# Kernel tuning notes

Hardware: AMD Instinct MI355X
Metric: run time of the kernel (lower is better)

The kernel has to match this reference:

```python
import jax, jax.numpy as jnp
import numpy as np

B, N, D, H = 16, 512, 256, 8
DK = D // H
EPS = 1e-6
NEG_INF = 1e12
LAM_ATT, LAM_DIST, LAM_ADJ = 0.3, 0.3, 0.4


def setup_inputs() -> dict:
    key = jax.random.key(0)
    ks = jax.random.split(key, 16)
    inp = {
        "query": jax.random.normal(ks[0], (B, N, D), jnp.float32),
        "key": jax.random.normal(ks[1], (B, N, D), jnp.float32),
        "value": jax.random.normal(ks[2], (B, N, D), jnp.float32),
        "adj_matrix": jax.random.uniform(ks[3], (B, N, N), jnp.float32),
        "distances_matrix": jax.random.uniform(ks[4], (B, N, N), jnp.float32),
        "edges_att": jnp.zeros((1,), jnp.float32),
        "mask": jnp.ones((B, N), jnp.int32),
    }
    s = 1.0 / np.sqrt(D)
    # four Linear(d_model, d_model): Wq, Wk, Wv, Wo (+ biases)
    for i, nm in enumerate(["q", "k", "v", "o"]):
        inp[f"W{nm}"] = jax.random.normal(ks[5 + 2 * i], (D, D), jnp.float32) * s
        inp[f"b{nm}"] = jax.random.normal(ks[6 + 2 * i], (D,), jnp.float32) * s
    return inp


def _proj(x, W, b):
    # [B,N,D] -> [B,H,N,DK]
    y = x @ W.T + b
    return y.reshape(B, N, H, DK).transpose(0, 2, 1, 3)


def reference(query, key, value, adj_matrix, distances_matrix, edges_att, mask,
              Wq, bq, Wk, bk, Wv, bv, Wo, bo):
    q = _proj(query, Wq, bq)
    k = _proj(key, Wk, bk)
    v = _proj(value, Wv, bv)

    valid = mask != 0  # [B,N] key-side validity

    # distance kernel: softmax(-d) over keys, masked positions -> 0 prob
    d_scores = jnp.where(valid[:, None, :], -distances_matrix, -jnp.inf)
    p_dist = jax.nn.softmax(d_scores, axis=-1)  # [B,N,N]

    # scaled dot-product attention with key mask
    scores = jnp.einsum("bhqd,bhkd->bhqk", q, k) / np.sqrt(DK)
    scores = jnp.where(valid[:, None, None, :], scores, -NEG_INF)
    p_attn = jax.nn.softmax(scores, axis=-1)  # [B,H,N,N]

    # row-normalized adjacency
    p_adj = adj_matrix / (adj_matrix.sum(axis=-1, keepdims=True) + EPS)  # [B,N,N]

    # blend three attention terms (broadcast dist/adj over heads)
    p_weighted = (LAM_ATT * p_attn
                  + LAM_DIST * p_dist[:, None]
                  + LAM_ADJ * p_adj[:, None])  # [B,H,N,N]

    x = jnp.einsum("bhqk,bhkd->bhqd", p_weighted, v)  # [B,H,N,DK]
    x = x.transpose(0, 2, 1, 3).reshape(B, N, D)
    out = x @ Wo.T + bo  # output projection (4th linear)
    return out
```

## Files before the change

kernel.cpp:

```cpp
#include <hip/hip_runtime.h>
#include <cstdint>
#include <cstddef>

#define B_  16
#define N_  512
#define D_  256
#define H_  8
#define DK_ 32

#define QKV_ELEMS 2097152

__device__ __align__(16) unsigned short g_Qb[QKV_ELEMS];
__device__ __align__(16) unsigned short g_Kb[QKV_ELEMS];
__device__ __align__(16) unsigned short g_VT[QKV_ELEMS];
__device__ __align__(16) unsigned short g_STb[(size_t)B_*N_*N_];
__device__ __align__(16) unsigned short g_Wb[4*D_*D_];

typedef short v8s __attribute__((ext_vector_type(8)));
typedef float v4f __attribute__((ext_vector_type(4)));

__device__ __forceinline__ unsigned short f2b(float f){
  unsigned int x;
  __builtin_memcpy(&x, &f, 4);
  x = x + 0x7FFFu + ((x >> 16) & 1u);
  return (unsigned short)(x >> 16);
}

#if defined(__has_builtin)
#if __has_builtin(__builtin_amdgcn_cvt_pk_bf16_f32)
#define PK_BF16 1
#endif
#endif

__device__ __forceinline__ unsigned int pk2(float a, float b){
#ifdef PK_BF16
  typedef __bf16 v2bf __attribute__((ext_vector_type(2)));
  v2bf r = __builtin_amdgcn_cvt_pk_bf16_f32(a, b);
  unsigned int u;
  __builtin_memcpy(&u, &r, 4);
  return u;
#else
  return (unsigned int)f2b(a) | ((unsigned int)f2b(b) << 16);
#endif
}
__device__ __forceinline__ v8s pk8(const float4 a, const float4 b){
  union { unsigned int u[4]; v8s v; } x;
  x.u[0] = pk2(a.x, a.y); x.u[1] = pk2(a.z, a.w);
  x.u[2] = pk2(b.x, b.y); x.u[3] = pk2(b.z, b.w);
  return x.v;
}

__global__ __launch_bounds__(256) void conv_w(
    const float* __restrict__ Wq, const float* __restrict__ Wk,
    const float* __restrict__ Wv, const float* __restrict__ Wo)
{
  const int widx = blockIdx.x >> 6;
  const int i = ((blockIdx.x & 63)*256 + threadIdx.x)*4;
  const float* src = (widx==0) ? Wq : (widx==1) ? Wk : (widx==2) ? Wv : Wo;
  const float4 u = *reinterpret_cast<const float4*>(src + i);
  uint2 o2;
  o2.x = pk2(u.x, u.y);
  o2.y = pk2(u.z, u.w);
  *reinterpret_cast<uint2*>(g_Wb + widx*65536 + i) = o2;
}

__global__ __launch_bounds__(256) void fused_mid(
    const float* __restrict__ query, const float* __restrict__ key_,
    const float* __restrict__ value, const float* __restrict__ dist,
    const float* __restrict__ adjm,  const int* __restrict__ mask,
    const float* __restrict__ bq, const float* __restrict__ bk,
    const float* __restrict__ bv)
{
  const int bid = blockIdx.x;
  const int t   = threadIdx.x;
  const int w = t >> 6, lane = t & 63, kl = lane & 15, quad = lane >> 4;

  if (bid < 1536){
    const int z  = bid >> 9;
    const int rr = bid & 511;
    const int mt = rr >> 2, nt = rr & 3;
    const float* Ap = (z==0) ? query : (z==1) ? key_ : value;
    const float* bp = (z==0) ? bq : (z==1) ? bk : bv;
    const unsigned short* Wb = g_Wb + z*65536;
    const int m0 = mt*64 + w*16;
    const int n0 = nt*64;

    v4f acc[4];
    #pragma unroll
    for (int nb = 0; nb < 4; ++nb) acc[nb] = (v4f){0.f,0.f,0.f,0.f};
    const int arow = m0 + kl;

    if (z == 2){
      #pragma unroll
      for (int k0 = 0; k0 < 256; k0 += 32){
        const float* ap = Ap + (size_t)arow*256 + k0 + quad*8;
        const v8s af = pk8(reinterpret_cast<const float4*>(ap)[0],
                           reinterpret_cast<const float4*>(ap)[1]);
        #pragma unroll
        for (int nb = 0; nb < 4; ++nb){
          const v8s wf = *reinterpret_cast<const v8s*>(
              Wb + (size_t)(n0 + nb*16 + kl)*256 + k0 + quad*8);
          acc[nb] = __builtin_amdgcn_mfma_f32_16x16x32_bf16(wf, af, acc[nb], 0, 0, 0);
        }
      }
      const int tok = m0 + kl, bb = tok >> 9, nr = tok & 511;
      #pragma unroll
      for (int nb = 0; nb < 4; ++nb)
        #pragma unroll
        for (int r = 0; r < 4; ++r){
          const int n = n0 + nb*16 + quad*4 + r;
          const float v = acc[nb][r] + bp[n];
          g_VT[(((size_t)bb*H_ + (n>>5))*DK_ + (n&31))*N_ + nr] = f2b(v);
        }
    } else {
      #pragma unroll
      for (int k0 = 0; k0 < 256; k0 += 32){
        const float* ap = Ap + (size_t)arow*256 + k0 + quad*8;
        const v8s af = pk8(reinterpret_cast<const float4*>(ap)[0],
                           reinterpret_cast<const float4*>(ap)[1]);
        #pragma unroll
        for (int nb = 0; nb < 4; ++nb){
          const v8s wf = *reinterpret_cast<const v8s*>(
              Wb + (size_t)(n0 + nb*16 + kl)*256 + k0 + quad*8);
          acc[nb] = __builtin_amdgcn_mfma_f32_16x16x32_bf16(af, wf, acc[nb], 0, 0, 0);
        }
      }
      unsigned short* dst = z ? g_Kb : g_Qb;
      #pragma unroll
      for (int nb = 0; nb < 4; ++nb){
        const int n = n0 + nb*16 + kl;
        const float bias = bp[n];
        #pragma unroll
        for (int r = 0; r < 4; ++r){
          const int m = m0 + quad*4 + r;
          const float v = acc[nb][r] + bias;
          dst[(((size_t)(m>>9)*H_ + (n>>5))*N_ + (m&511))*DK_ + (n&31)] = f2b(v);
        }
      }
    }
    return;
  }

  {
    const int row = (bid - 1536)*4 + w;
    const int b   = row >> 9;
    const size_t roff = (size_t)row*N_ + lane*8;
    const float4 d0 = *reinterpret_cast<const float4*>(dist + roff);
    const float4 d1 = *reinterpret_cast<const float4*>(dist + roff + 4);
    const float4 a0 = *reinterpret_cast<const float4*>(adjm + roff);
    const float4 a1 = *reinterpret_cast<const float4*>(adjm + roff + 4);
    const int4   m0v = *reinterpret_cast<const int4*>(mask + b*N_ + lane*8);
    const int4   m1v = *reinterpret_cast<const int4*>(mask + b*N_ + lane*8 + 4);
    float e[8], a[8];
    e[0] = m0v.x ? __expf(-d0.x) : 0.f;  e[1] = m0v.y ? __expf(-d0.y) : 0.f;
    e[2] = m0v.z ? __expf(-d0.z) : 0.f;  e[3] = m0v.w ? __expf(-d0.w) : 0.f;
    e[4] = m1v.x ? __expf(-d1.x) : 0.f;  e[5] = m1v.y ? __expf(-d1.y) : 0.f;
    e[6] = m1v.z ? __expf(-d1.z) : 0.f;  e[7] = m1v.w ? __expf(-d1.w) : 0.f;
    a[0]=a0.x; a[1]=a0.y; a[2]=a0.z; a[3]=a0.w;
    a[4]=a1.x; a[5]=a1.y; a[6]=a1.z; a[7]=a1.w;
    float lz = 0.f, la = 0.f;
    #pragma unroll
    for (int i = 0; i < 8; ++i){ lz += e[i]; la += a[i]; }
    #pragma unroll
    for (int o = 1; o < 64; o <<= 1){
      lz += __shfl_xor(lz, o, 64);
      la += __shfl_xor(la, o, 64);
    }
    const float c0 = (lz > 0.f) ? 0.3f / lz : 0.f;
    const float c1 = 0.4f / (la + 1e-6f);
    uint4 o4;
    o4.x = pk2(e[0]*c0 + a[0]*c1, e[1]*c0 + a[1]*c1);
    o4.y = pk2(e[2]*c0 + a[2]*c1, e[3]*c0 + a[3]*c1);
    o4.z = pk2(e[4]*c0 + a[4]*c1, e[5]*c0 + a[5]*c1);
    o4.w = pk2(e[6]*c0 + a[6]*c1, e[7]*c0 + a[7]*c1);
    *reinterpret_cast<uint4*>(g_STb + roff) = o4;
  }
}

__global__ __launch_bounds__(512) void attn_kernel(
    const int* __restrict__ mask, const float* __restrict__ bo,
    float* __restrict__ out)
{
  __shared__ unsigned short Pl[8*2*640];
  __shared__ unsigned short Xl[16*264];
  const int bid = blockIdx.x;
  const int b  = bid & 15;
  const int qt = bid >> 4;
  const int q0 = qt*16;
  const int t  = threadIdx.x;
  const int w  = t >> 6, lane = t & 63;
  const int kl = lane & 15, quad = lane >> 4;
  const int h  = w;
  const size_t bh = (size_t)b*H_ + h;
  const float scale = 0.17677669529663687f;

  const unsigned short* Qp = g_Qb + (bh*N_ + q0)*DK_;
  const unsigned short* Kp = g_Kb + bh*N_*DK_;
  const unsigned short* Vp = g_VT + bh*DK_*N_;
  const unsigned short* Sp = g_STb + ((size_t)(b*N_ + q0))*N_;
  const int* mrow = mask + b*N_;
  const v4f vz = {0.f, 0.f, 0.f, 0.f};

  const v8s aq = *reinterpret_cast<const v8s*>(Qp + (size_t)kl*DK_ + quad*8);

  v4f acc[32];
  #pragma unroll
  for (int kb = 0; kb < 32; ++kb){
    const v8s ak = *reinterpret_cast<const v8s*>(Kp + (size_t)(kb*16 + kl)*DK_ + quad*8);
    acc[kb] = __builtin_amdgcn_mfma_f32_16x16x32_bf16(ak, aq, vz, 0, 0, 0);
  }

  float psum = 0.f;
  #pragma unroll
  for (int kb = 0; kb < 32; ++kb){
    const int4 mv = reinterpret_cast<const int4*>(mrow + kb*16)[quad];
    acc[kb][0] = mv.x ? __expf(acc[kb][0]*scale) : 0.f;
    acc[kb][1] = mv.y ? __expf(acc[kb][1]*scale) : 0.f;
    acc[kb][2] = mv.z ? __expf(acc[kb][2]*scale) : 0.f;
    acc[kb][3] = mv.w ? __expf(acc[kb][3]*scale) : 0.f;
    psum += (acc[kb][0] + acc[kb][1]) + (acc[kb][2] + acc[kb][3]);
  }
  psum += __shfl_xor(psum, 16, 64);
  psum += __shfl_xor(psum, 32, 64);
  const float inv = (psum > 0.f) ? 0.3f / psum : 0.f;

  unsigned short* Pw = Pl + w*1280;
  v4f o0 = vz, o1 = vz;
  #pragma unroll
  for (int c = 0; c < 16; ++c){
    unsigned short* Pb = Pw + (c & 1)*640;
    {
      union { unsigned int u[2]; unsigned long long ll; } p0, p1;
      p0.u[0] = pk2(acc[2*c  ][0]*inv, acc[2*c  ][1]*inv);
      p0.u[1] = pk2(acc[2*c  ][2]*inv, acc[2*c  ][3]*inv);
      p1.u[0] = pk2(acc[2*c+1][0]*inv, acc[2*c+1][1]*inv);
      p1.u[1] = pk2(acc[2*c+1][2]*inv, acc[2*c+1][3]*inv);
      *reinterpret_cast<unsigned long long*>(&Pb[kl*40 + quad*4])      = p0.ll;
      *reinterpret_cast<unsigned long long*>(&Pb[kl*40 + 16 + quad*4]) = p1.ll;
    }
    const v8s bp  = *reinterpret_cast<const v8s*>(&Pb[kl*40 + quad*8]);
    const v8s bst = *reinterpret_cast<const v8s*>(Sp + (size_t)kl*N_ + c*32 + quad*8);
    const v8s av0 = *reinterpret_cast<const v8s*>(Vp + (size_t)(     kl)*N_ + c*32 + quad*8);
    const v8s av1 = *reinterpret_cast<const v8s*>(Vp + (size_t)(16 + kl)*N_ + c*32 + quad*8);
    o0 = __builtin_amdgcn_mfma_f32_16x16x32_bf16(av0, bp,  o0, 0, 0, 0);
    o0 = __builtin_amdgcn_mfma_f32_16x16x32_bf16(av0, bst, o0, 0, 0, 0);
    o1 = __builtin_amdgcn_mfma_f32_16x16x32_bf16(av1, bp,  o1, 0, 0, 0);
    o1 = __builtin_amdgcn_mfma_f32_16x16x32_bf16(av1, bst, o1, 0, 0, 0);
  }

  {
    unsigned short* xr = Xl + kl*264 + h*32;
    *reinterpret_cast<unsigned int*>(&xr[quad*4])          = pk2(o0[0], o0[1]);
    *reinterpret_cast<unsigned int*>(&xr[quad*4 + 2])      = pk2(o0[2], o0[3]);
    *reinterpret_cast<unsigned int*>(&xr[16 + quad*4])     = pk2(o1[0], o1[1]);
    *reinterpret_cast<unsigned int*>(&xr[16 + quad*4 + 2]) = pk2(o1[2], o1[3]);
  }
  __syncthreads();

  {
    const unsigned short* WoB = g_Wb + 3*65536;
    const int n0 = w*32;
    v4f a20 = vz, a21 = vz;
    #pragma unroll
    for (int k0 = 0; k0 < 256; k0 += 32){
      const v8s af  = *reinterpret_cast<const v8s*>(&Xl[kl*264 + k0 + quad*8]);
      const v8s wf0 = *reinterpret_cast<const v8s*>(WoB + (size_t)(n0 + kl)*256 + k0 + quad*8);
      const v8s wf1 = *reinterpret_cast<const v8s*>(WoB + (size_t)(n0 + 16 + kl)*256 + k0 + quad*8);
      a20 = __builtin_amdgcn_mfma_f32_16x16x32_bf16(af, wf0, a20, 0, 0, 0);
      a21 = __builtin_amdgcn_mfma_f32_16x16x32_bf16(af, wf1, a21, 0, 0, 0);
    }
    const int n_0 = n0 + kl, n_1 = n0 + 16 + kl;
    const float b0v = bo[n_0], b1v = bo[n_1];
    #pragma unroll
    for (int r = 0; r < 4; ++r){
      const size_t m = (size_t)(b*N_ + q0 + quad*4 + r);
      out[m*256 + n_0] = a20[r] + b0v;
      out[m*256 + n_1] = a21[r] + b1v;
    }
  }
}

extern "C" void kernel_launch(void* const* d_in, const int* in_sizes, int n_in,
                              void* d_out, int out_size, void* d_ws, size_t ws_size,
                              hipStream_t stream)
{
  const float* query = (const float*)d_in[0];
  const float* key_  = (const float*)d_in[1];
  const float* value = (const float*)d_in[2];
  const float* adjm  = (const float*)d_in[3];
  const float* dist  = (const float*)d_in[4];
  const int*   mask  = (const int*)d_in[6];
  const float* Wq = (const float*)d_in[7];  const float* bq = (const float*)d_in[8];
  const float* Wk = (const float*)d_in[9];  const float* bk = (const float*)d_in[10];
  const float* Wv = (const float*)d_in[11]; const float* bv = (const float*)d_in[12];
  const float* Wo = (const float*)d_in[13]; const float* bo = (const float*)d_in[14];

  conv_w<<<256, 256, 0, stream>>>(Wq, Wk, Wv, Wo);
  fused_mid<<<3584, 256, 0, stream>>>(query, key_, value, dist, adjm, mask,
                                      bq, bk, bv);
  attn_kernel<<<512, 512, 0, stream>>>(mask, bo, (float*)d_out);
}
```

Measured before the change: 198.1 us.

## Drop weight-conversion kernel and stream attention softmax with hi/lo bf16 split

Removes the separate conv_w launch. Q/K/V weights are now read as fp32 and packed to bf16 inside the projection GEMM, and Wo conversion runs as extra blocks of fused_mid. In attn_kernel the 32-tile score array held in registers is replaced by a single streaming pass. Unnormalized exp scores are split into bf16 hi and lo parts and fed through extra MFMAs, with normalization applied at the end and the static term accumulated separately. This cuts a launch and register pressure at the cost of redundant weight conversion and more MFMA and LDS work per tile.

New measurement: 216.8 us. +9.5%, slower.

```diff
diff --git a/kernel.cpp b/kernel.cpp
--- a/kernel.cpp
+++ b/kernel.cpp
@@ -14,9 +14,10 @@
 __device__ __align__(16) unsigned short g_Kb[QKV_ELEMS];
 __device__ __align__(16) unsigned short g_VT[QKV_ELEMS];
 __device__ __align__(16) unsigned short g_STb[(size_t)B_*N_*N_];
-__device__ __align__(16) unsigned short g_Wb[4*D_*D_];
+__device__ __align__(16) unsigned short g_WoB[D_*D_];
 
 typedef short v8s __attribute__((ext_vector_type(8)));
+typedef short v4s __attribute__((ext_vector_type(4)));
 typedef float v4f __attribute__((ext_vector_type(4)));
 
 __device__ __forceinline__ unsigned short f2b(float f){
@@ -49,25 +50,21 @@
   x.u[2] = pk2(b.x, b.y); x.u[3] = pk2(b.z, b.w);
   return x.v;
 }
-
-__global__ __launch_bounds__(256) void conv_w(
-    const float* __restrict__ Wq, const float* __restrict__ Wk,
-    const float* __restrict__ Wv, const float* __restrict__ Wo)
-{
-  const int widx = blockIdx.x >> 6;
-  const int i = ((blockIdx.x & 63)*256 + threadIdx.x)*4;
-  const float* src = (widx==0) ? Wq : (widx==1) ? Wk : (widx==2) ? Wv : Wo;
-  const float4 u = *reinterpret_cast<const float4*>(src + i);
-  uint2 o2;
-  o2.x = pk2(u.x, u.y);
-  o2.y = pk2(u.z, u.w);
-  *reinterpret_cast<uint2*>(g_Wb + widx*65536 + i) = o2;
+__device__ __forceinline__ float lo16f(unsigned int u){
+  const unsigned int x = u << 16;
+  float f; __builtin_memcpy(&f, &x, 4); return f;
+}
+__device__ __forceinline__ float hi16f(unsigned int u){
+  const unsigned int x = u & 0xFFFF0000u;
+  float f; __builtin_memcpy(&f, &x, 4); return f;
 }
 
 __global__ __launch_bounds__(256) void fused_mid(
     const float* __restrict__ query, const float* __restrict__ key_,
     const float* __restrict__ value, const float* __restrict__ dist,
     const float* __restrict__ adjm,  const int* __restrict__ mask,
+    const float* __restrict__ Wq, const float* __restrict__ Wk,
+    const float* __restrict__ Wv, const float* __restrict__ Wo,
     const float* __restrict__ bq, const float* __restrict__ bk,
     const float* __restrict__ bv)
 {
@@ -80,8 +77,8 @@
     const int rr = bid & 511;
     const int mt = rr >> 2, nt = rr & 3;
     const float* Ap = (z==0) ? query : (z==1) ? key_ : value;
+    const float* Wp = (z==0) ? Wq : (z==1) ? Wk : Wv;
     const float* bp = (z==0) ? bq : (z==1) ? bk : bv;
-    const unsigned short* Wb = g_Wb + z*65536;
     const int m0 = mt*64 + w*16;
     const int n0 = nt*64;
 
@@ -90,19 +87,24 @@
     for (int nb = 0; nb < 4; ++nb) acc[nb] = (v4f){0.f,0.f,0.f,0.f};
     const int arow = m0 + kl;
 
+    #pragma unroll
+    for (int k0 = 0; k0 < 256; k0 += 32){
+      const float* ap = Ap + (size_t)arow*256 + k0 + quad*8;
+      const v8s af = pk8(reinterpret_cast<const float4*>(ap)[0],
+                         reinterpret_cast<const float4*>(ap)[1]);
+      #pragma unroll
+      for (int nb = 0; nb < 4; ++nb){
+        const float* wp = Wp + (size_t)(n0 + nb*16 + kl)*256 + k0 + quad*8;
+        const v8s wf = pk8(reinterpret_cast<const float4*>(wp)[0],
+                           reinterpret_cast<const float4*>(wp)[1]);
+        if (z == 2)
+          acc[nb] = __builtin_amdgcn_mfma_f32_16x16x32_bf16(wf, af, acc[nb], 0, 0, 0);
+        else
+          acc[nb] = __builtin_amdgcn_mfma_f32_16x16x32_bf16(af, wf, acc[nb], 0, 0, 0);
+      }
+    }
+
     if (z == 2){
-      #pragma unroll
-      for (int k0 = 0; k0 < 256; k0 += 32){
-        const float* ap = Ap + (size_t)arow*256 + k0 + quad*8;
-        const v8s af = pk8(reinterpret_cast<const float4*>(ap)[0],
-                           reinterpret_cast<const float4*>(ap)[1]);
-        #pragma unroll
-        for (int nb = 0; nb < 4; ++nb){
-          const v8s wf = *reinterpret_cast<const v8s*>(
-              Wb + (size_t)(n0 + nb*16 + kl)*256 + k0 + quad*8);
-          acc[nb] = __builtin_amdgcn_mfma_f32_16x16x32_bf16(wf, af, acc[nb], 0, 0, 0);
-        }
-      }
       const int tok = m0 + kl, bb = tok >> 9, nr = tok & 511;
       #pragma unroll
       for (int nb = 0; nb < 4; ++nb)
@@ -113,18 +115,6 @@
           g_VT[(((size_t)bb*H_ + (n>>5))*DK_ + (n&31))*N_ + nr] = f2b(v);
         }
     } else {
-      #pragma unroll
-      for (int k0 = 0; k0 < 256; k0 += 32){
-        const float* ap = Ap + (size_t)arow*256 + k0 + quad*8;
-        const v8s af = pk8(reinterpret_cast<const float4*>(ap)[0],
-                           reinterpret_cast<const float4*>(ap)[1]);
-        #pragma unroll
-        for (int nb = 0; nb < 4; ++nb){
-          const v8s wf = *reinterpret_cast<const v8s*>(
-              Wb + (size_t)(n0 + nb*16 + kl)*256 + k0 + quad*8);
-          acc[nb] = __builtin_amdgcn_mfma_f32_16x16x32_bf16(af, wf, acc[nb], 0, 0, 0);
-        }
-      }
       unsigned short* dst = z ? g_Kb : g_Qb;
       #pragma unroll
       for (int nb = 0; nb < 4; ++nb){
@@ -141,7 +131,7 @@
     return;
   }
 
-  {
+  if (bid < 3584){
     const int row = (bid - 1536)*4 + w;
     const int b   = row >> 9;
     const size_t roff = (size_t)row*N_ + lane*8;
@@ -174,6 +164,16 @@
     o4.z = pk2(e[4]*c0 + a[4]*c1, e[5]*c0 + a[5]*c1);
     o4.w = pk2(e[6]*c0 + a[6]*c1, e[7]*c0 + a[7]*c1);
     *reinterpret_cast<uint4*>(g_STb + roff) = o4;
+    return;
+  }
+
+  {
+    const int i = ((bid - 3584)*256 + t)*4;
+    const float4 u = *reinterpret_cast<const float4*>(Wo + i);
+    uint2 o2;
+    o2.x = pk2(u.x, u.y);
+    o2.y = pk2(u.z, u.w);
+    *reinterpret_cast<uint2*>(g_WoB + i) = o2;
   }
 }
 
@@ -181,7 +181,7 @@
     const int* __restrict__ mask, const float* __restrict__ bo,
     float* __restrict__ out)
 {
-  __shared__ unsigned short Pl[8*2*640];
+  __shared__ unsigned short Pl[8*16*80];
   __shared__ unsigned short Xl[16*264];
   const int bid = blockIdx.x;
   const int b  = bid & 15;
@@ -203,49 +203,70 @@
 
   const v8s aq = *reinterpret_cast<const v8s*>(Qp + (size_t)kl*DK_ + quad*8);
 
-  v4f acc[32];
+  unsigned short* Pw = Pl + w*1280;
+  v4f o0 = vz, o1 = vz;
+  v4f s0 = vz, s1 = vz;
+  float psum = 0.f;
+
   #pragma unroll
-  for (int kb = 0; kb < 32; ++kb){
-    const v8s ak = *reinterpret_cast<const v8s*>(Kp + (size_t)(kb*16 + kl)*DK_ + quad*8);
-    acc[kb] = __builtin_amdgcn_mfma_f32_16x16x32_bf16(ak, aq, vz, 0, 0, 0);
-  }
-
-  float psum = 0.f;
-  #pragma unroll
-  for (int kb = 0; kb < 32; ++kb){
-    const int4 mv = reinterpret_cast<const int4*>(mrow + kb*16)[quad];
-    acc[kb][0] = mv.x ? __expf(acc[kb][0]*scale) : 0.f;
-    acc[kb][1] = mv.y ? __expf(acc[kb][1]*scale) : 0.f;
-    acc[kb][2] = mv.z ? __expf(acc[kb][2]*scale) : 0.f;
-    acc[kb][3] = mv.w ? __expf(acc[kb][3]*scale) : 0.f;
-    psum += (acc[kb][0] + acc[kb][1]) + (acc[kb][2] + acc[kb][3]);
-  }
+  for (int c = 0; c < 16; ++c){
+    const v8s ak0 = *reinterpret_cast<const v8s*>(Kp + (size_t)(c*32 +      kl)*DK_ + quad*8);
+    const v8s ak1 = *reinterpret_cast<const v8s*>(Kp + (size_t)(c*32 + 16 + kl)*DK_ + quad*8);
+    v4f t0 = __builtin_amdgcn_mfma_f32_16x16x32_bf16(ak0, aq, vz, 0, 0, 0);
+    v4f t1 = __builtin_amdgcn_mfma_f32_16x16x32_bf16(ak1, aq, vz, 0, 0, 0);
+
+    const int4 mv0 = reinterpret_cast<const int4*>(mrow + c*32)[quad];
+    const int4 mv1 = reinterpret_cast<const int4*>(mrow + c*32 + 16)[quad];
+    t0[0] = mv0.x ? __expf(t0[0]*scale) : 0.f;
+    t0[1] = mv0.y ? __expf(t0[1]*scale) : 0.f;
+    t0[2] = mv0.z ? __expf(t0[2]*scale) : 0.f;
+    t0[3] = mv0.w ? __expf(t0[3]*scale) : 0.f;
+    t1[0] = mv1.x ? __expf(t1[0]*scale) : 0.f;
+    t1[1] = mv1.y ? __expf(t1[1]*scale) : 0.f;
+    t1[2] = mv1.z ? __expf(t1[2]*scale) : 0.f;
+    t1[3] = mv1.w ? __expf(t1[3]*scale) : 0.f;
+    psum += (t0[0]+t0[1]) + (t0[2]+t0[3]) + (t1[0]+t1[1]) + (t1[2]+t1[3]);
+
+    const unsigned int h00 = pk2(t0[0], t0[1]);
+    const unsigned int h01 = pk2(t0[2], t0[3]);
+    const unsigned int h10 = pk2(t1[0], t1[1]);
+    const unsigned int h11 = pk2(t1[2], t1[3]);
+    const unsigned int l00 = pk2(t0[0] - lo16f(h00), t0[1] - hi16f(h00));
+    const unsigned int l01 = pk2(t0[2] - lo16f(h01), t0[3] - hi16f(h01));
+    const unsigned int l10 = pk2(t1[0] - lo16f(h10), t1[1] - hi16f(h10));
+    const unsigned int l11 = pk2(t1[2] - lo16f(h11), t1[3] - hi16f(h11));
+
+    {
+      union { unsigned int u[2]; v4s v; } wv;
+      wv.u[0] = h00; wv.u[1] = h01;
+      *reinterpret_cast<v4s*>(&Pw[kl*80 + quad*4])      = wv.v;
+      wv.u[0] = h10; wv.u[1] = h11;
+      *reinterpret_cast<v4s*>(&Pw[kl*80 + 16 + quad*4]) = wv.v;
+      wv.u[0] = l00; wv.u[1] = l01;
+      *reinterpret_cast<v4s*>(&Pw[kl*80 + 40 + quad*4])      = wv.v;
+      wv.u[0] = l10; wv.u[1] = l11;
+      *reinterpret_cast<v4s*>(&Pw[kl*80 + 40 + 16 + quad*4]) = wv.v;
+    }
+    const v8s bph = *reinterpret_cast<const v8s*>(&Pw[kl*80 + quad*8]);
+    const v8s bpl = *reinterpret_cast<const v8s*>(&Pw[kl*80 + 40 + quad*8]);
+    const v8s bst = *reinterpret_cast<const v8s*>(Sp + (size_t)kl*N_ + c*32 + quad*8);
+    const v8s av0 = *reinterpret_cast<const v8s*>(Vp + (size_t)(     kl)*N_ + c*32 + quad*8);
+    const v8s av1 = *reinterpret_cast<const v8s*>(Vp + (size_t)(16 + kl)*N_ + c*32 + quad*8);
+    o0 = __builtin_amdgcn_mfma_f32_16x16x32_bf16(av0, bph, o0, 0, 0, 0);
+    o0 = __builtin_amdgcn_mfma_f32_16x16x32_bf16(av0, bpl, o0, 0, 0, 0);
+    s0 = __builtin_amdgcn_mfma_f32_16x16x32_bf16(av0, bst, s0, 0, 0, 0);
+    o1 = __builtin_amdgcn_mfma_f32_16x16x32_bf16(av1, bph, o1, 0, 0, 0);
+    o1 = __builtin_amdgcn_mfma_f32_16x16x32_bf16(av1, bpl, o1, 0, 0, 0);
+    s1 = __builtin_amdgcn_mfma_f32_16x16x32_bf16(av1, bst, s1, 0, 0, 0);
+  }
+
   psum += __shfl_xor(psum, 16, 64);
   psum += __shfl_xor(psum, 32, 64);
   const float inv = (psum > 0.f) ? 0.3f / psum : 0.f;
-
-  unsigned short* Pw = Pl + w*1280;
-  v4f o0 = vz, o1 = vz;
   #pragma unroll
-  for (int c = 0; c < 16; ++c){
-    unsigned short* Pb = Pw + (c & 1)*640;
-    {
-      union { unsigned int u[2]; unsigned long long ll; } p0, p1;
-      p0.u[0] = pk2(acc[2*c  ][0]*inv, acc[2*c  ][1]*inv);
-      p0.u[1] = pk2(acc[2*c  ][2]*inv, acc[2*c  ][3]*inv);
-      p1.u[0] = pk2(acc[2*c+1][0]*inv, acc[2*c+1][1]*inv);
-      p1.u[1] = pk2(acc[2*c+1][2]*inv, acc[2*c+1][3]*inv);
-      *reinterpret_cast<unsigned long long*>(&Pb[kl*40 + quad*4])      = p0.ll;
-      *reinterpret_cast<unsigned long long*>(&Pb[kl*40 + 16 + quad*4]) = p1.ll;
-    }
-    const v8s bp  = *reinterpret_cast<const v8s*>(&Pb[kl*40 + quad*8]);
-    const v8s bst = *reinterpret_cast<const v8s*>(Sp + (size_t)kl*N_ + c*32 + quad*8);
-    const v8s av0 = *reinterpret_cast<const v8s*>(Vp + (size_t)(     kl)*N_ + c*32 + quad*8);
-    const v8s av1 = *reinterpret_cast<const v8s*>(Vp + (size_t)(16 + kl)*N_ + c*32 + quad*8);
-    o0 = __builtin_amdgcn_mfma_f32_16x16x32_bf16(av0, bp,  o0, 0, 0, 0);
-    o0 = __builtin_amdgcn_mfma_f32_16x16x32_bf16(av0, bst, o0, 0, 0, 0);
-    o1 = __builtin_amdgcn_mfma_f32_16x16x32_bf16(av1, bp,  o1, 0, 0, 0);
-    o1 = __builtin_amdgcn_mfma_f32_16x16x32_bf16(av1, bst, o1, 0, 0, 0);
+  for (int r = 0; r < 4; ++r){
+    o0[r] = o0[r]*inv + s0[r];
+    o1[r] = o1[r]*inv + s1[r];
   }
 
   {
@@ -258,14 +279,13 @@
   __syncthreads();
 
   {
-    const unsigned short* WoB = g_Wb + 3*65536;
     const int n0 = w*32;
     v4f a20 = vz, a21 = vz;
     #pragma unroll
     for (int k0 = 0; k0 < 256; k0 += 32){
       const v8s af  = *reinterpret_cast<const v8s*>(&Xl[kl*264 + k0 + quad*8]);
-      const v8s wf0 = *reinterpret_cast<const v8s*>(WoB + (size_t)(n0 + kl)*256 + k0 + quad*8);
-      const v8s wf1 = *reinterpret_cast<const v8s*>(WoB + (size_t)(n0 + 16 + kl)*256 + k0 + quad*8);
+      const v8s wf0 = *reinterpret_cast<const v8s*>(g_WoB + (size_t)(n0 + kl)*256 + k0 + quad*8);
+      const v8s wf1 = *reinterpret_cast<const v8s*>(g_WoB + (size_t)(n0 + 16 + kl)*256 + k0 + quad*8);
       a20 = __builtin_amdgcn_mfma_f32_16x16x32_bf16(af, wf0, a20, 0, 0, 0);
       a21 = __builtin_amdgcn_mfma_f32_16x16x32_bf16(af, wf1, a21, 0, 0, 0);
     }
@@ -295,8 +315,7 @@
   const float* Wv = (const float*)d_in[11]; const float* bv = (const float*)d_in[12];
   const float* Wo = (const float*)d_in[13]; const float* bo = (const float*)d_in[14];
 
-  conv_w<<<256, 256, 0, stream>>>(Wq, Wk, Wv, Wo);
-  fused_mid<<<3584, 256, 0, stream>>>(query, key_, value, dist, adjm, mask,
-                                      bq, bk, bv);
+  fused_mid<<<3648, 256, 0, stream>>>(query, key_, value, dist, adjm, mask,
+                                      Wq, Wk, Wv, Wo, bq, bk, bv);
   attn_kernel<<<512, 512, 0, stream>>>(mask, bo, (float*)d_out);
 }
```
